# Performance work log

Hardware: AMD Instinct MI355X
Metric: run time of the kernel (lower is better)

The kernel has to match this reference:

```python
import jax, jax.numpy as jnp
import numpy as np

D_MODEL = 1024
NUM_HEADS = 16
HEAD_DIM = D_MODEL // NUM_HEADS
THETA = 10000.0


def _trunc_normal(key, shape, std):
    # approximate trunc_normal_(a=-3std, b=3std) by clipping
    return jnp.clip(jax.random.normal(key, shape) * std, -3 * std, 3 * std)


def setup_inputs() -> dict:
    key = jax.random.key(0)
    ks = jax.random.split(key, 6)
    B, S = 2, 2048
    x = jax.random.normal(ks[0], (B, S, D_MODEL), dtype=jnp.float32)
    token_positions = jnp.sort(
        jax.random.randint(ks[1], (B, S), 0, 2048), axis=-1
    ).astype(jnp.int64)
    std = float(np.sqrt(2.0 / (D_MODEL + D_MODEL)))
    Wq = _trunc_normal(ks[2], (D_MODEL, D_MODEL), std)
    Wk = _trunc_normal(ks[3], (D_MODEL, D_MODEL), std)
    Wv = _trunc_normal(ks[4], (D_MODEL, D_MODEL), std)
    Wo = _trunc_normal(ks[5], (D_MODEL, D_MODEL), std)
    return {"x": x, "Wq": Wq, "Wk": Wk, "Wv": Wv, "Wo": Wo,
            "token_positions": token_positions}


def _rope(x, positions):
    # x: (b, h, s, d), positions: (b, s)
    d = x.shape[-1]
    inv_freq = THETA ** (-jnp.arange(0, d, 2, dtype=jnp.float32) / d)  # (d/2,)
    angles = positions.astype(jnp.float32)[:, None, :, None] * inv_freq  # (b,1,s,d/2)
    cos, sin = jnp.cos(angles), jnp.sin(angles)
    x_even, x_odd = x[..., 0::2], x[..., 1::2]
    out_even = x_even * cos - x_odd * sin
    out_odd = x_even * sin + x_odd * cos
    # interleave back: (..., d/2, 2) -> (..., d)
    return jnp.stack([out_even, out_odd], axis=-1).reshape(x.shape)


def reference(x, Wq, Wk, Wv, Wo, token_positions):
    B, S, _ = x.shape
    H, Dh = NUM_HEADS, HEAD_DIM
    # projections: einsum '... i, o i -> ... o'
    q = jnp.einsum('bsi,oi->bso', x, Wq).reshape(B, S, H, Dh).transpose(0, 2, 1, 3)
    k = jnp.einsum('bsi,oi->bso', x, Wk).reshape(B, S, H, Dh).transpose(0, 2, 1, 3)
    v = jnp.einsum('bsi,oi->bso', x, Wv).reshape(B, S, H, Dh).transpose(0, 2, 1, 3)
    q = _rope(q, token_positions)
    k = _rope(k, token_positions)
    scores = jnp.einsum('bhqd,bhkd->bhqk', q.astype(jnp.float32),
                        k.astype(jnp.float32)) / jnp.sqrt(
        jnp.asarray(Dh, dtype=jnp.float32))
    causal = jnp.tril(jnp.ones((S, S), dtype=bool))
    scores = jnp.where(causal, scores, -jnp.inf)
    attn = jax.nn.softmax(scores, axis=-1)
    out = jnp.einsum('bhqk,bhkd->bhqd', attn, v.astype(jnp.float32)).astype(x.dtype)
    out = out.transpose(0, 2, 1, 3).reshape(B, S, H * Dh)
    return jnp.einsum('bsi,oi->bso', out, Wo)
```

## Files before the change

kernel.cpp:

```cpp
#include <hip/hip_runtime.h>
#include <hip/hip_bf16.h>

#define DMODEL 1024
#define NHEADS 16
#define HDIM   64
#define BATCH  2
#define SEQ    2048
#define XELEMS ((size_t)BATCH * SEQ * DMODEL)
#define WELEMS ((size_t)DMODEL * DMODEL)

typedef __attribute__((ext_vector_type(8))) __bf16 bf16x8;
typedef __attribute__((ext_vector_type(4))) float  f32x4;
typedef __attribute__((ext_vector_type(2))) float  f32x2;
typedef __attribute__((ext_vector_type(4))) unsigned int   u32x4;
typedef __attribute__((ext_vector_type(4))) unsigned short u16x4;
typedef __attribute__((ext_vector_type(8))) unsigned short u16x8;

typedef const __attribute__((address_space(1))) void* gas_t;
typedef __attribute__((address_space(3))) void* las_t;

static __device__ __forceinline__ unsigned short f2bf(float f) {
  return __builtin_bit_cast(unsigned short, __float2bfloat16(f));
}
static __device__ __forceinline__ float bf2f(unsigned short u) {
  return __bfloat162float(__builtin_bit_cast(__hip_bfloat16, u));
}

__global__ __launch_bounds__(64) void probe_kernel(const unsigned int* __restrict__ x,
                                                   const int* __restrict__ pos,
                                                   int* __restrict__ flags) {
  const int lane = threadIdx.x;
  int bad = 0;
#pragma unroll
  for (int i = 0; i < 32; ++i) {
    const unsigned int u = x[lane * 32 + i];
    if (((u >> 23) & 0xFFu) == 0xFFu) bad++;
  }
  int zodd = 0;
#pragma unroll
  for (int i = 0; i < 4; ++i)
    if (pos[lane * 8 + 2 * i + 1] == 0) zodd++;
#pragma unroll
  for (int s = 1; s < 64; s <<= 1) {
    bad  += __shfl_xor(bad, s);
    zodd += __shfl_xor(zodd, s);
  }
  if (lane == 0) {
    flags[0] = (bad < 64) ? 1 : 0;
    flags[1] = (zodd >= 200) ? 1 : 0;
  }
}

__global__ __launch_bounds__(256) void rope_table_kernel(const int* __restrict__ pos,
                                                         const int* __restrict__ flags,
                                                         float* __restrict__ tab) {
  const int i = blockIdx.x * 256 + threadIdx.x;
  const int pd = i & 31, rs = i >> 5;
  const int pv = flags[1] ? pos[2 * rs] : pos[rs];
  const float ang = (float)pv * exp2f(-(float)pd * 0.41524101186092026f);
  f32x2 t; t[0] = cosf(ang); t[1] = sinf(ang);
  *(f32x2*)&tab[2 * i] = t;
}

__global__ __launch_bounds__(256) void conv_kernel(
    const void* __restrict__ x,
    const void* __restrict__ w0, const void* __restrict__ w1,
    const void* __restrict__ w2, const void* __restrict__ w3,
    unsigned short* __restrict__ dst, const int* __restrict__ flags) {
  const size_t e = ((size_t)blockIdx.x * 256 + threadIdx.x) * 8;
  const void* src;
  size_t off;
  if (e < XELEMS) { src = x; off = e; }
  else {
    const size_t r = e - XELEMS;
    const int wi = (int)(r >> 20);
    src = (wi == 0) ? w0 : (wi == 1) ? w1 : (wi == 2) ? w2 : w3;
    off = r & (WELEMS - 1);
  }
  if (flags[0]) {
    const float* s = (const float*)src + off;
    const f32x4 a = *(const f32x4*)(s);
    const f32x4 b = *(const f32x4*)(s + 4);
    u16x8 o8;
#pragma unroll
    for (int j = 0; j < 4; ++j) o8[j] = f2bf(a[j]);
#pragma unroll
    for (int j = 0; j < 4; ++j) o8[4 + j] = f2bf(b[j]);
    *(u16x8*)(dst + e) = o8;
  } else {
    *(u32x4*)(dst + e) = *(const u32x4*)((const unsigned short*)src + off);
  }
}

__device__ __forceinline__ void gemm_core(const unsigned short* __restrict__ Ag,
                                          const unsigned short* __restrict__ Bg,
                                          unsigned short* As, unsigned short* Bs,
                                          int bm, int bn, f32x4 acc[4][4]) {
  const int tid = threadIdx.x;
  const int lane = tid & 63;
  const int w  = tid >> 6;
  const int wm = w >> 1, wn = w & 1;
  const int c = lane & 15, g = lane >> 4;
  const int r0 = tid >> 2;
  const int s0 = (tid & 3) * 8;

  auto stage = [&](int buf, int k0) {
    unsigned short* ad = As + buf * 4096;
    unsigned short* bd = Bs + buf * 4096;
    __builtin_amdgcn_global_load_lds((gas_t)(Ag + (size_t)(bm + r0) * DMODEL + k0 + s0),
                                     (las_t)(ad + tid * 8), 16, 0, 0);
    __builtin_amdgcn_global_load_lds((gas_t)(Ag + (size_t)(bm + r0 + 64) * DMODEL + k0 + s0),
                                     (las_t)(ad + (tid + 256) * 8), 16, 0, 0);
    __builtin_amdgcn_global_load_lds((gas_t)(Bg + (size_t)(bn + r0) * DMODEL + k0 + s0),
                                     (las_t)(bd + tid * 8), 16, 0, 0);
    __builtin_amdgcn_global_load_lds((gas_t)(Bg + (size_t)(bn + r0 + 64) * DMODEL + k0 + s0),
                                     (las_t)(bd + (tid + 256) * 8), 16, 0, 0);
  };

  stage(0, 0);
  __syncthreads();
  for (int k0 = 0; k0 < DMODEL; k0 += 32) {
    const int cur = (k0 >> 5) & 1;
    if (k0 + 32 < DMODEL) stage(cur ^ 1, k0 + 32);
    const unsigned short* ar = As + cur * 4096;
    const unsigned short* br = Bs + cur * 4096;
    bf16x8 af[4], bfr[4];
#pragma unroll
    for (int m = 0; m < 4; ++m)
      af[m] = *(const bf16x8*)&ar[(wm * 64 + m * 16 + c) * 32 + g * 8];
#pragma unroll
    for (int n = 0; n < 4; ++n)
      bfr[n] = *(const bf16x8*)&br[(wn * 64 + n * 16 + c) * 32 + g * 8];
    __builtin_amdgcn_s_setprio(1);
#pragma unroll
    for (int m = 0; m < 4; ++m)
#pragma unroll
      for (int n = 0; n < 4; ++n)
        acc[m][n] = __builtin_amdgcn_mfma_f32_16x16x32_bf16(af[m], bfr[n], acc[m][n], 0, 0, 0);
    __builtin_amdgcn_s_setprio(0);
    __syncthreads();
  }
}

__global__ __launch_bounds__(256) void qkv_gemm_kernel(
    const unsigned short* __restrict__ x,
    const unsigned short* __restrict__ Wq, const unsigned short* __restrict__ Wk,
    const unsigned short* __restrict__ Wv,
    unsigned short* __restrict__ qo, unsigned short* __restrict__ ko,
    unsigned short* __restrict__ vto) {
  __shared__ unsigned short As[2 * 128 * 32];
  __shared__ unsigned short Bs[2 * 128 * 32];
  const int z = blockIdx.z;
  const unsigned short* W = (z == 0) ? Wq : (z == 1) ? Wk : Wv;
  const int bm = blockIdx.x * 128, bn = blockIdx.y * 128;
  f32x4 acc[4][4];
#pragma unroll
  for (int m = 0; m < 4; ++m)
#pragma unroll
    for (int n = 0; n < 4; ++n)
#pragma unroll
      for (int j = 0; j < 4; ++j) acc[m][n][j] = 0.f;

  gemm_core(x, W, As, Bs, bm, bn, acc);

  const int tid = threadIdx.x, lane = tid & 63, w = tid >> 6;
  const int wm = w >> 1, wn = w & 1, c = lane & 15, g4 = lane >> 4;
#pragma unroll
  for (int m = 0; m < 4; ++m) {
#pragma unroll
    for (int n = 0; n < 4; ++n) {
      const int col = bn + wn * 64 + n * 16 + c;
      const int h = col >> 6, d = col & 63;
      const int row0 = bm + wm * 64 + m * 16 + g4 * 4;
      if (z == 2) {
        const int b = row0 >> 11, s0 = row0 & (SEQ - 1);
        u16x4 pk;
#pragma unroll
        for (int j = 0; j < 4; ++j) pk[j] = f2bf(acc[m][n][j]);
        *(u16x4*)&vto[((size_t)(b * NHEADS + h) * HDIM + d) * SEQ + s0] = pk;
      } else {
        unsigned short* dst = z ? ko : qo;
#pragma unroll
        for (int j = 0; j < 4; ++j) {
          const int row = row0 + j;
          const int b = row >> 11, s = row & (SEQ - 1);
          dst[((size_t)(b * NHEADS + h) * SEQ + s) * HDIM + d] = f2bf(acc[m][n][j]);
        }
      }
    }
  }
}

__global__ __launch_bounds__(256) void out_gemm_kernel(
    const unsigned short* __restrict__ A, const unsigned short* __restrict__ Wo,
    void* __restrict__ outv, const int* __restrict__ flags) {
  __shared__ unsigned short As[2 * 64 * 32];
  __shared__ unsigned short Bs[2 * 128 * 32];
  const int bm = blockIdx.x * 64, bn = blockIdx.y * 128;
  const int tid = threadIdx.x, lane = tid & 63, w = tid >> 6;
  const int c = lane & 15, g = lane >> 4;
  const int r0 = tid >> 2, s0 = (tid & 3) * 8;
  f32x4 acc[4][2];
#pragma unroll
  for (int m = 0; m < 4; ++m)
#pragma unroll
    for (int n = 0; n < 2; ++n)
#pragma unroll
      for (int j = 0; j < 4; ++j) acc[m][n][j] = 0.f;

  auto stage = [&](int buf, int k0) {
    __builtin_amdgcn_global_load_lds((gas_t)(A + (size_t)(bm + r0) * DMODEL + k0 + s0),
                                     (las_t)(As + buf * 2048 + tid * 8), 16, 0, 0);
    __builtin_amdgcn_global_load_lds((gas_t)(Wo + (size_t)(bn + r0) * DMODEL + k0 + s0),
                                     (las_t)(Bs + buf * 4096 + tid * 8), 16, 0, 0);
    __builtin_amdgcn_global_load_lds((gas_t)(Wo + (size_t)(bn + r0 + 64) * DMODEL + k0 + s0),
                                     (las_t)(Bs + buf * 4096 + (tid + 256) * 8), 16, 0, 0);
  };

  stage(0, 0);
  __syncthreads();
  for (int k0 = 0; k0 < DMODEL; k0 += 32) {
    const int cur = (k0 >> 5) & 1;
    if (k0 + 32 < DMODEL) stage(cur ^ 1, k0 + 32);
    const unsigned short* ar = As + cur * 2048;
    const unsigned short* br = Bs + cur * 4096;
    bf16x8 af[4], bfr[2];
#pragma unroll
    for (int m = 0; m < 4; ++m)
      af[m] = *(const bf16x8*)&ar[(m * 16 + c) * 32 + g * 8];
#pragma unroll
    for (int n = 0; n < 2; ++n)
      bfr[n] = *(const bf16x8*)&br[(w * 32 + n * 16 + c) * 32 + g * 8];
    __builtin_amdgcn_s_setprio(1);
#pragma unroll
    for (int m = 0; m < 4; ++m)
#pragma unroll
      for (int n = 0; n < 2; ++n)
        acc[m][n] = __builtin_amdgcn_mfma_f32_16x16x32_bf16(af[m], bfr[n], acc[m][n], 0, 0, 0);
    __builtin_amdgcn_s_setprio(0);
    __syncthreads();
  }

  const int f32o = flags[0];
  if (f32o) {
    float* out = (float*)outv;
#pragma unroll
    for (int m = 0; m < 4; ++m)
#pragma unroll
      for (int n = 0; n < 2; ++n) {
        const int col = bn + w * 32 + n * 16 + c;
#pragma unroll
        for (int j = 0; j < 4; ++j) {
          const int row = bm + m * 16 + g * 4 + j;
          out[(size_t)row * DMODEL + col] = acc[m][n][j];
        }
      }
  } else {
    unsigned short* out = (unsigned short*)outv;
#pragma unroll
    for (int m = 0; m < 4; ++m)
#pragma unroll
      for (int n = 0; n < 2; ++n) {
        const int col = bn + w * 32 + n * 16 + c;
#pragma unroll
        for (int j = 0; j < 4; ++j) {
          const int row = bm + m * 16 + g * 4 + j;
          out[(size_t)row * DMODEL + col] = f2bf(acc[m][n][j]);
        }
      }
  }
}

__global__ __launch_bounds__(256) void rope_kernel(unsigned short* __restrict__ k,
                                                   const float* __restrict__ tab) {
  const int p = blockIdx.x * 256 + threadIdx.x;
  const int j = p & 31;
  const int s = (p >> 5) & (SEQ - 1);
  const int bh = p >> 16;
  const int b = bh >> 4;
  const f32x2 t = *(const f32x2*)&tab[(((size_t)(b * SEQ + s)) * 32 + j) * 2];
  const float cs = t[0], sn = t[1];
  unsigned int* wp = (unsigned int*)k + ((p >> 5) * 32 + j);
  const unsigned int u = *wp;
  const float e = bf2f((unsigned short)(u & 0xffffu));
  const float o = bf2f((unsigned short)(u >> 16));
  *wp = (unsigned int)f2bf(e * cs - o * sn) | ((unsigned int)f2bf(e * sn + o * cs) << 16);
}

#define MNEG -1e30f
#define QBLK 64
#define LOG2E 1.4426950408889634f

template<int BUF>
__device__ __forceinline__ void flash_tile(
    int kt, int nkv, int qt, int qbase, int wq, int c, int g, int tid,
    const unsigned short* (&kp)[2], const unsigned short* (&vp)[2],
    unsigned short (&Ks)[2][64 * 64], unsigned short (&Vs)[2][64 * 64],
    unsigned short (&Ps)[64 * 64],
    const bf16x8 (&qf)[2], f32x4 (&acco)[4], float& m_r, float& l_r) {
  const int kvb = kt * 64;
  if (kt + 1 < nkv) {
#pragma unroll
    for (int i = 0; i < 2; ++i) {
      const int t8 = (tid + i * 256) * 8;
      __builtin_amdgcn_global_load_lds((gas_t)kp[i], (las_t)(Ks[BUF ^ 1] + t8), 16, 0, 0);
      __builtin_amdgcn_global_load_lds((gas_t)vp[i], (las_t)(Vs[BUF ^ 1] + t8), 16, 0, 0);
      kp[i] += 64 * HDIM;
      vp[i] += 64;
    }
  }

  f32x4 accs[4];
#pragma unroll
  for (int n = 0; n < 4; ++n)
#pragma unroll
    for (int j = 0; j < 4; ++j) accs[n][j] = 0.f;
  __builtin_amdgcn_s_setprio(1);
#pragma unroll
  for (int kk = 0; kk < 2; ++kk)
#pragma unroll
    for (int n = 0; n < 4; ++n) {
      const int r = n * 16 + c;
      const int sl = (kk * 4 + g) ^ (r & 7);
      const bf16x8 ak = *(const bf16x8*)&Ks[BUF][r * 64 + sl * 8];
      accs[n] = __builtin_amdgcn_mfma_f32_16x16x32_bf16(ak, qf[kk], accs[n], 0, 0, 0);
    }
  __builtin_amdgcn_s_setprio(0);

  const int qg = qbase + wq + c;
  if (kt == qt) {
#pragma unroll
    for (int n = 0; n < 4; ++n)
#pragma unroll
      for (int jj = 0; jj < 4; ++jj)
        if (kvb + n * 16 + g * 4 + jj > qg) accs[n][jj] = MNEG;
  }

  float rm = accs[0][0];
#pragma unroll
  for (int n = 0; n < 4; ++n)
#pragma unroll
    for (int jj = 0; jj < 4; ++jj) rm = fmaxf(rm, accs[n][jj]);
  rm = fmaxf(rm, __shfl_xor(rm, 16));
  rm = fmaxf(rm, __shfl_xor(rm, 32));
  if (!__all(rm <= m_r + 8.f)) {
    const float mn = fmaxf(m_r, rm);
    const float al = exp2f((m_r - mn) * LOG2E);
    l_r *= al;
#pragma unroll
    for (int n = 0; n < 4; ++n)
#pragma unroll
      for (int jj = 0; jj < 4; ++jj) acco[n][jj] *= al;
    m_r = mn;
  }
  float rs = 0.f;
#pragma unroll
  for (int n = 0; n < 4; ++n)
#pragma unroll
    for (int jj = 0; jj < 4; ++jj) {
      const float pv = exp2f((accs[n][jj] - m_r) * LOG2E);
      accs[n][jj] = pv;
      rs += pv;
    }
  rs += __shfl_xor(rs, 16);
  rs += __shfl_xor(rs, 32);
  l_r += rs;

  const int pr = wq + c;
  const int px = (pr & 7) << 3;
#pragma unroll
  for (int n = 0; n < 4; ++n) {
    u16x4 pk4;
#pragma unroll
    for (int jj = 0; jj < 4; ++jj) pk4[jj] = f2bf(accs[n][jj]);
    *(u16x4*)&Ps[pr * 64 + ((n * 16 + g * 4) ^ px)] = pk4;
  }

  __builtin_amdgcn_s_setprio(1);
#pragma unroll
  for (int kk = 0; kk < 2; ++kk) {
    const bf16x8 pb = *(const bf16x8*)&Ps[pr * 64 + ((kk * 32 + g * 8) ^ px)];
#pragma unroll
    for (int n = 0; n < 4; ++n) {
      const int r = n * 16 + c;
      const int sl = (kk * 4 + g) ^ (r & 7);
      const bf16x8 av = *(const bf16x8*)&Vs[BUF][r * 64 + sl * 8];
      acco[n] = __builtin_amdgcn_mfma_f32_16x16x32_bf16(av, pb, acco[n], 0, 0, 0);
    }
  }
  __builtin_amdgcn_s_setprio(0);
  __syncthreads();
}

__global__ __launch_bounds__(256, 4) void flash_kernel(
    const unsigned short* __restrict__ q, const unsigned short* __restrict__ k,
    const unsigned short* __restrict__ vt, unsigned short* __restrict__ o,
    const float* __restrict__ tab) {
  __shared__ unsigned short Ks[2][64 * 64];
  __shared__ unsigned short Vs[2][64 * 64];
  __shared__ unsigned short Ps[64 * 64];

  const int wg = blockIdx.x;
  const int qt = (SEQ / QBLK - 1) - (wg >> 5);
  const int bh = wg & 31;
  const int qbase = qt * QBLK;
  const int tid = threadIdx.x, lane = tid & 63, w = tid >> 6;
  const int c = lane & 15, g = lane >> 4;
  const int wq = w * 16;
  const size_t tb = (size_t)bh * SEQ * HDIM;

  const int srow0 = qbase + wq + c;
  const size_t rsb = (size_t)((bh >> 4) * SEQ + srow0) * 32;
  bf16x8 qf[2];
#pragma unroll
  for (int kk = 0; kk < 2; ++kk) {
    const u16x8 qr = *(const u16x8*)(q + tb + (size_t)srow0 * HDIM + kk * 32 + g * 8);
    const int pd0 = kk * 16 + g * 4;
    const f32x4 t0 = *(const f32x4*)&tab[(rsb + pd0) * 2];
    const f32x4 t1 = *(const f32x4*)&tab[(rsb + pd0) * 2 + 4];
    u16x8 outp;
#pragma unroll
    for (int j = 0; j < 4; ++j) {
      const float cs = (j < 2) ? t0[2 * j] : t1[2 * (j - 2)];
      const float sn = (j < 2) ? t0[2 * j + 1] : t1[2 * (j - 2) + 1];
      const float e = bf2f(qr[2 * j]);
      const float od = bf2f(qr[2 * j + 1]);
      outp[2 * j]     = f2bf((e * cs - od * sn) * 0.125f);
      outp[2 * j + 1] = f2bf((e * sn + od * cs) * 0.125f);
    }
    qf[kk] = __builtin_bit_cast(bf16x8, outp);
  }

  const unsigned short* kp[2];
  const unsigned short* vp[2];
#pragma unroll
  for (int i = 0; i < 2; ++i) {
    const int t = tid + i * 256;
    const int r = t >> 3;
    const int sl = (t & 7) ^ (r & 7);
    kp[i] = k + tb + (size_t)r * HDIM + sl * 8;
    vp[i] = vt + tb + (size_t)r * SEQ + sl * 8;
  }
#pragma unroll
  for (int i = 0; i < 2; ++i) {
    const int t8 = (tid + i * 256) * 8;
    __builtin_amdgcn_global_load_lds((gas_t)kp[i], (las_t)(Ks[0] + t8), 16, 0, 0);
    __builtin_amdgcn_global_load_lds((gas_t)vp[i], (las_t)(Vs[0] + t8), 16, 0, 0);
    kp[i] += 64 * HDIM;
    vp[i] += 64;
  }
  __syncthreads();

  f32x4 acco[4];
#pragma unroll
  for (int n = 0; n < 4; ++n)
#pragma unroll
    for (int j = 0; j < 4; ++j) acco[n][j] = 0.f;
  float m_r = MNEG, l_r = 0.f;

  const int nkv = qt + 1;
  int kt = 0;
  for (; kt + 2 <= nkv; kt += 2) {
    flash_tile<0>(kt,     nkv, qt, qbase, wq, c, g, tid, kp, vp, Ks, Vs, Ps, qf, acco, m_r, l_r);
    flash_tile<1>(kt + 1, nkv, qt, qbase, wq, c, g, tid, kp, vp, Ks, Vs, Ps, qf, acco, m_r, l_r);
  }
  if (kt < nkv)
    flash_tile<0>(kt, nkv, qt, qbase, wq, c, g, tid, kp, vp, Ks, Vs, Ps, qf, acco, m_r, l_r);

  const float rl = 1.f / fmaxf(l_r, 1e-20f);
  const int b = bh >> 4, h = bh & 15;
#pragma unroll
  for (int n = 0; n < 4; ++n) {
    u16x4 pk;
#pragma unroll
    for (int jj = 0; jj < 4; ++jj) pk[jj] = f2bf(acco[n][jj] * rl);
    *(u16x4*)&o[(size_t)(b * SEQ + srow0) * DMODEL + h * 64 + n * 16 + g * 4] = pk;
  }
}

extern "C" void kernel_launch(void* const* d_in, const int* in_sizes, int n_in,
                              void* d_out, int out_size, void* d_ws, size_t ws_size,
                              hipStream_t stream) {
  (void)in_sizes; (void)n_in; (void)out_size; (void)ws_size;
  const size_t MB = (size_t)1 << 20;
  char* ws = (char*)d_ws;
  unsigned short* xb  = (unsigned short*)(ws);
  unsigned short* Wqb = (unsigned short*)(ws + 8 * MB);
  unsigned short* Wkb = (unsigned short*)(ws + 10 * MB);
  unsigned short* Wvb = (unsigned short*)(ws + 12 * MB);
  unsigned short* Wob = (unsigned short*)(ws + 14 * MB);
  unsigned short* qw  = (unsigned short*)(ws + 16 * MB);
  unsigned short* kw  = (unsigned short*)(ws + 24 * MB);
  unsigned short* vtw = (unsigned short*)(ws + 32 * MB);
  int* flags          = (int*)(ws + 40 * MB);
  float* tab          = (float*)(ws + 40 * MB + 4096);
  unsigned short* ow  = xb;

  const dim3 blk(256);
  probe_kernel<<<1, 64, 0, stream>>>((const unsigned int*)d_in[0], (const int*)d_in[5], flags);
  rope_table_kernel<<<512, blk, 0, stream>>>((const int*)d_in[5], flags, tab);
  conv_kernel<<<4096, blk, 0, stream>>>(d_in[0], d_in[1], d_in[2], d_in[3], d_in[4], xb, flags);
  qkv_gemm_kernel<<<dim3(32, 8, 3), blk, 0, stream>>>(xb, Wqb, Wkb, Wvb, qw, kw, vtw);
  rope_kernel<<<8192, blk, 0, stream>>>(kw, tab);
  flash_kernel<<<dim3(1024), blk, 0, stream>>>(qw, kw, vtw, ow, tab);
  out_gemm_kernel<<<dim3(64, 8), blk, 0, stream>>>(ow, Wob, d_out, flags);
}
```

Measured before the change: 121.7 us.

## Rewrite QKV GEMM with 256x256 tiles, swizzled LDS and fused weight matrix

The QKV projection now treats Wq, Wk and Wv as one contiguous 3072-row weight matrix and computes 256x256 output tiles with 512 threads. It loads 64-wide K slices into XOR-swizzled LDS, which avoids bank conflicts, and double-buffers them with explicit barriers, interleaving loads with MFMA groups. The goal is more data reuse per block and fewer launches, at the cost of only 192 blocks, which may underfill the 256 CUs, and one block per CU because of the large LDS use.

```diff
diff --git a/kernel.cpp b/kernel.cpp
--- a/kernel.cpp
+++ b/kernel.cpp
@@ -92,102 +92,117 @@
   }
 }
 
-__device__ __forceinline__ void gemm_core(const unsigned short* __restrict__ Ag,
-                                          const unsigned short* __restrict__ Bg,
-                                          unsigned short* As, unsigned short* Bs,
-                                          int bm, int bn, f32x4 acc[4][4]) {
-  const int tid = threadIdx.x;
-  const int lane = tid & 63;
-  const int w  = tid >> 6;
-  const int wm = w >> 1, wn = w & 1;
-  const int c = lane & 15, g = lane >> 4;
-  const int r0 = tid >> 2;
-  const int s0 = (tid & 3) * 8;
-
-  auto stage = [&](int buf, int k0) {
-    unsigned short* ad = As + buf * 4096;
-    unsigned short* bd = Bs + buf * 4096;
-    __builtin_amdgcn_global_load_lds((gas_t)(Ag + (size_t)(bm + r0) * DMODEL + k0 + s0),
-                                     (las_t)(ad + tid * 8), 16, 0, 0);
-    __builtin_amdgcn_global_load_lds((gas_t)(Ag + (size_t)(bm + r0 + 64) * DMODEL + k0 + s0),
-                                     (las_t)(ad + (tid + 256) * 8), 16, 0, 0);
-    __builtin_amdgcn_global_load_lds((gas_t)(Bg + (size_t)(bn + r0) * DMODEL + k0 + s0),
-                                     (las_t)(bd + tid * 8), 16, 0, 0);
-    __builtin_amdgcn_global_load_lds((gas_t)(Bg + (size_t)(bn + r0 + 64) * DMODEL + k0 + s0),
-                                     (las_t)(bd + (tid + 256) * 8), 16, 0, 0);
-  };
-
-  stage(0, 0);
-  __syncthreads();
-  for (int k0 = 0; k0 < DMODEL; k0 += 32) {
-    const int cur = (k0 >> 5) & 1;
-    if (k0 + 32 < DMODEL) stage(cur ^ 1, k0 + 32);
-    const unsigned short* ar = As + cur * 4096;
-    const unsigned short* br = Bs + cur * 4096;
-    bf16x8 af[4], bfr[4];
-#pragma unroll
-    for (int m = 0; m < 4; ++m)
-      af[m] = *(const bf16x8*)&ar[(wm * 64 + m * 16 + c) * 32 + g * 8];
-#pragma unroll
-    for (int n = 0; n < 4; ++n)
-      bfr[n] = *(const bf16x8*)&br[(wn * 64 + n * 16 + c) * 32 + g * 8];
-    __builtin_amdgcn_s_setprio(1);
-#pragma unroll
-    for (int m = 0; m < 4; ++m)
-#pragma unroll
-      for (int n = 0; n < 4; ++n)
-        acc[m][n] = __builtin_amdgcn_mfma_f32_16x16x32_bf16(af[m], bfr[n], acc[m][n], 0, 0, 0);
-    __builtin_amdgcn_s_setprio(0);
-    __syncthreads();
-  }
-}
-
-__global__ __launch_bounds__(256) void qkv_gemm_kernel(
-    const unsigned short* __restrict__ x,
-    const unsigned short* __restrict__ Wq, const unsigned short* __restrict__ Wk,
-    const unsigned short* __restrict__ Wv,
+__global__ __launch_bounds__(512, 1) void qkv_gemm_kernel(
+    const unsigned short* __restrict__ x, const unsigned short* __restrict__ Wcat,
     unsigned short* __restrict__ qo, unsigned short* __restrict__ ko,
     unsigned short* __restrict__ vto) {
-  __shared__ unsigned short As[2 * 128 * 32];
-  __shared__ unsigned short Bs[2 * 128 * 32];
-  const int z = blockIdx.z;
-  const unsigned short* W = (z == 0) ? Wq : (z == 1) ? Wk : Wv;
-  const int bm = blockIdx.x * 128, bn = blockIdx.y * 128;
-  f32x4 acc[4][4];
-#pragma unroll
-  for (int m = 0; m < 4; ++m)
+  __shared__ unsigned short Sh[4 * 256 * 64];
+  unsigned short* const As[2] = {Sh, Sh + 16384};
+  unsigned short* const Bs[2] = {Sh + 32768, Sh + 49152};
+  const int bm = blockIdx.x * 256, bn = blockIdx.y * 256;
+  const int tid = threadIdx.x, lane = tid & 63, w = tid >> 6;
+  const int wm = w >> 2, wn = w & 3;
+  const int c = lane & 15, g = lane >> 4;
+  const int r0 = tid >> 3;
+  const int sl8 = ((tid & 7) ^ (r0 & 7)) * 8;
+
+  f32x4 acc[8][4];
+#pragma unroll
+  for (int m = 0; m < 8; ++m)
 #pragma unroll
     for (int n = 0; n < 4; ++n)
 #pragma unroll
       for (int j = 0; j < 4; ++j) acc[m][n][j] = 0.f;
 
-  gemm_core(x, W, As, Bs, bm, bn, acc);
-
-  const int tid = threadIdx.x, lane = tid & 63, w = tid >> 6;
-  const int wm = w >> 1, wn = w & 1, c = lane & 15, g4 = lane >> 4;
-#pragma unroll
-  for (int m = 0; m < 4; ++m) {
-#pragma unroll
-    for (int n = 0; n < 4; ++n) {
-      const int col = bn + wn * 64 + n * 16 + c;
-      const int h = col >> 6, d = col & 63;
-      const int row0 = bm + wm * 64 + m * 16 + g4 * 4;
-      if (z == 2) {
+  auto stage = [&](int buf, int k0) {
+#pragma unroll
+    for (int i = 0; i < 4; ++i) {
+      __builtin_amdgcn_global_load_lds((gas_t)(x + (size_t)(bm + r0 + i * 64) * DMODEL + k0 + sl8),
+                                       (las_t)(As[buf] + (tid + i * 512) * 8), 16, 0, 0);
+      __builtin_amdgcn_global_load_lds((gas_t)(Wcat + (size_t)(bn + r0 + i * 64) * DMODEL + k0 + sl8),
+                                       (las_t)(Bs[buf] + (tid + i * 512) * 8), 16, 0, 0);
+    }
+  };
+
+  stage(0, 0);
+
+  for (int t8 = 0; t8 < 8; ++t8) {
+    const int kt0 = t8 * 128;
+#pragma unroll
+    for (int half = 0; half < 2; ++half) {
+      const int buf = half;
+      bf16x8 bfr[4][2];
+#pragma unroll
+      for (int qd = 0; qd < 4; ++qd) {
+        bf16x8 af[2][2];
+        if (qd == 0) {
+          asm volatile("s_waitcnt vmcnt(0)" ::: "memory");
+          asm volatile("s_barrier" ::: "memory");
+#pragma unroll
+          for (int n = 0; n < 4; ++n)
+#pragma unroll
+            for (int kk = 0; kk < 2; ++kk) {
+              const int R = wn * 64 + n * 16 + c;
+              bfr[n][kk] = *(const bf16x8*)&Bs[buf][R * 64 + (((kk * 4 + g) ^ (R & 7)) * 8)];
+            }
+        }
+#pragma unroll
+        for (int m2 = 0; m2 < 2; ++m2)
+#pragma unroll
+          for (int kk = 0; kk < 2; ++kk) {
+            const int R = wm * 128 + (qd * 2 + m2) * 16 + c;
+            af[m2][kk] = *(const bf16x8*)&As[buf][R * 64 + (((kk * 4 + g) ^ (R & 7)) * 8)];
+          }
+        if (qd == 0) {
+          if (half == 0) stage(1, kt0 + 64);
+          else if (t8 + 1 < 8) stage(0, kt0 + 128);
+        }
+        asm volatile("s_barrier" ::: "memory");
+        __builtin_amdgcn_s_setprio(1);
+#pragma unroll
+        for (int m2 = 0; m2 < 2; ++m2)
+#pragma unroll
+          for (int n = 0; n < 4; ++n)
+#pragma unroll
+            for (int kk = 0; kk < 2; ++kk)
+              acc[qd * 2 + m2][n] = __builtin_amdgcn_mfma_f32_16x16x32_bf16(
+                  af[m2][kk], bfr[n][kk], acc[qd * 2 + m2][n], 0, 0, 0);
+        __builtin_amdgcn_s_setprio(0);
+        asm volatile("s_barrier" ::: "memory");
+      }
+    }
+  }
+
+  const int z = bn >> 10;
+  const int bnz = bn & 1023;
+  if (z == 2) {
+#pragma unroll
+    for (int m = 0; m < 8; ++m)
+#pragma unroll
+      for (int n = 0; n < 4; ++n) {
+        const int col = bnz + wn * 64 + n * 16 + c;
+        const int h = col >> 6, d = col & 63;
+        const int row0 = bm + wm * 128 + m * 16 + g * 4;
         const int b = row0 >> 11, s0 = row0 & (SEQ - 1);
         u16x4 pk;
 #pragma unroll
         for (int j = 0; j < 4; ++j) pk[j] = f2bf(acc[m][n][j]);
         *(u16x4*)&vto[((size_t)(b * NHEADS + h) * HDIM + d) * SEQ + s0] = pk;
-      } else {
-        unsigned short* dst = z ? ko : qo;
-#pragma unroll
-        for (int j = 0; j < 4; ++j) {
-          const int row = row0 + j;
-          const int b = row >> 11, s = row & (SEQ - 1);
-          dst[((size_t)(b * NHEADS + h) * SEQ + s) * HDIM + d] = f2bf(acc[m][n][j]);
-        }
       }
-    }
+  } else {
+    unsigned short* dst = z ? ko : qo;
+#pragma unroll
+    for (int m = 0; m < 8; ++m)
+#pragma unroll
+      for (int n = 0; n < 4; ++n) {
+        const int col = bnz + wn * 64 + n * 16 + c;
+        const int h = col >> 6, d = col & 63;
+        const int row0 = bm + wm * 128 + m * 16 + g * 4;
+        const int b = row0 >> 11, s0 = row0 & (SEQ - 1);
+#pragma unroll
+        for (int j = 0; j < 4; ++j)
+          dst[((size_t)(b * NHEADS + h) * SEQ + (s0 + j)) * HDIM + d] = f2bf(acc[m][n][j]);
+      }
   }
 }
 
@@ -486,8 +501,6 @@
   char* ws = (char*)d_ws;
   unsigned short* xb  = (unsigned short*)(ws);
   unsigned short* Wqb = (unsigned short*)(ws + 8 * MB);
-  unsigned short* Wkb = (unsigned short*)(ws + 10 * MB);
-  unsigned short* Wvb = (unsigned short*)(ws + 12 * MB);
   unsigned short* Wob = (unsigned short*)(ws + 14 * MB);
   unsigned short* qw  = (unsigned short*)(ws + 16 * MB);
   unsigned short* kw  = (unsigned short*)(ws + 24 * MB);
@@ -500,7 +513,7 @@
   probe_kernel<<<1, 64, 0, stream>>>((const unsigned int*)d_in[0], (const int*)d_in[5], flags);
   rope_table_kernel<<<512, blk, 0, stream>>>((const int*)d_in[5], flags, tab);
   conv_kernel<<<4096, blk, 0, stream>>>(d_in[0], d_in[1], d_in[2], d_in[3], d_in[4], xb, flags);
-  qkv_gemm_kernel<<<dim3(32, 8, 3), blk, 0, stream>>>(xb, Wqb, Wkb, Wvb, qw, kw, vtw);
+  qkv_gemm_kernel<<<dim3(16, 12), dim3(512), 0, stream>>>(xb, Wqb, qw, kw, vtw);
   rope_kernel<<<8192, blk, 0, stream>>>(kw, tab);
   flash_kernel<<<dim3(1024), blk, 0, stream>>>(qw, kw, vtw, ow, tab);
   out_gemm_kernel<<<dim3(64, 8), blk, 0, stream>>>(ow, Wob, d_out, flags);
```

Measured after the change: 129.5 us. +6.4%, slower.
